# Optimization experiments

Measured on AMD Instinct MI355X. Metric: run time of the kernel, lower is better.

The kernel has to match this reference:

```python
import jax, jax.numpy as jnp
import numpy as np

SCALING = 2.0      # lora_alpha / r = 32 / 16
TEMPERATURE = 1.0  # router_temperature


def setup_inputs() -> dict:
    key = jax.random.key(0)
    ks = jax.random.split(key, 7)
    B, S, D, K, R = 4, 2048, 4096, 8, 16
    # Note: torch inits lora_B to zeros; we use small random values so the
    return {
        "x": jax.random.normal(ks[0], (B, S, D), dtype=jnp.float32),
        "base_w": jax.random.normal(ks[1], (D, D), dtype=jnp.float32) * 0.02,
        "base_b": jax.random.normal(ks[2], (D,), dtype=jnp.float32) * 0.02,
        "lora_A": jax.random.normal(ks[3], (K, R, D), dtype=jnp.float32) * 0.02,
        "lora_B": jax.random.normal(ks[4], (K, D, R), dtype=jnp.float32) * 0.02,
        "router_w": jax.random.normal(ks[5], (K, D), dtype=jnp.float32) * 0.02,
        "router_b": jnp.zeros((K,), dtype=jnp.float32),
    }


def reference(x, base_w, base_b, lora_A, lora_B, router_w, router_b):
    # base_layer(x): x @ W^T + b
    base = jnp.einsum("bsd,od->bso", x, base_w) + base_b
    # router on mean-pooled sequence (x.dim()==3 branch): softmax(Linear(mean_s x))
    router_in = x.mean(axis=1)                                   # [B, D]
    logits = router_in @ router_w.T + router_b                   # [B, K]
    weights = jax.nn.softmax(logits / TEMPERATURE, axis=-1)      # [B, K]
    # grouped LoRA experts: h = A_k x, out = sum_k w_k * B_k h  (dropout p=0 -> identity)
    h = jnp.einsum("bsd,krd->bskr", x, lora_A)                   # [B, S, K, R]
    lora = jnp.einsum("bskr,kor,bk->bso", h, lora_B, weights)    # [B, S, D]
    return base + SCALING * lora
```

## Files before the change

kernel.cpp:

```cpp
#include <hip/hip_runtime.h>
#include <hip/hip_fp16.h>
#include <stdint.h>

typedef _Float16 f16;
typedef __attribute__((ext_vector_type(8))) _Float16 f16x8;
typedef __attribute__((ext_vector_type(4))) float f32x4;

#define D_DIM 4096
#define S_DIM 2048
#define M_DIM 8192
#define R_DIM 16
#define KR 128
#define KTOT 4224
#define SCALING 2.0f

#define WS_AP    0
#define WS_WP    69206016
#define WS_AH    103809024
#define WS_HP    104857600
#define WS_CS    121634816
#define WS_LG    121700352
#define WS_WS    121700480

__device__ __forceinline__ void load_lds16(const void* g, void* l) {
  __builtin_amdgcn_global_load_lds(
      (const __attribute__((address_space(1))) void*)g,
      (__attribute__((address_space(3))) void*)l, 16, 0, 0);
}

union H4 { f16 h[4]; ushort4 u; };

__global__ void conv_x(const float* __restrict__ x, f16* __restrict__ Ap,
                       float* __restrict__ colsum) {
  int rc = blockIdx.x;
  int cc = blockIdx.y;
  int col = cc * 1024 + threadIdx.x * 4;
  long base = (long)rc * 64 * D_DIM + col;
  float s0 = 0, s1 = 0, s2 = 0, s3 = 0;
  for (int r = 0; r < 64; ++r) {
    float4 v = *(const float4*)(x + base + (long)r * D_DIM);
    H4 t; t.h[0] = (f16)v.x; t.h[1] = (f16)v.y; t.h[2] = (f16)v.z; t.h[3] = (f16)v.w;
    *(ushort4*)((char*)Ap + ((long)(rc * 64 + r) * KTOT + col) * 2) = t.u;
    s0 += v.x; s1 += v.y; s2 += v.z; s3 += v.w;
  }
  int b = rc >> 5;
  float* cs = colsum + b * D_DIM + col;
  atomicAdd(cs + 0, s0); atomicAdd(cs + 1, s1);
  atomicAdd(cs + 2, s2); atomicAdd(cs + 3, s3);
}

__global__ void conv_w(const float* __restrict__ w, f16* __restrict__ Wp) {
  int rc = blockIdx.x;
  int cc = blockIdx.y;
  int col = cc * 1024 + threadIdx.x * 4;
  long base = (long)rc * 64 * D_DIM + col;
  for (int r = 0; r < 64; ++r) {
    float4 v = *(const float4*)(w + base + (long)r * D_DIM);
    H4 t; t.h[0] = (f16)v.x; t.h[1] = (f16)v.y; t.h[2] = (f16)v.z; t.h[3] = (f16)v.w;
    *(ushort4*)((char*)Wp + ((long)(rc * 64 + r) * KTOT + col) * 2) = t.u;
  }
}

__global__ void conv_bext(const float* __restrict__ loraB, f16* __restrict__ Wp) {
  int g = blockIdx.x * 256 + threadIdx.x;
  int n = g >> 7, kr = g & 127;
  int k = kr >> 4, r = kr & 15;
  float v = loraB[((long)k * D_DIM + n) * R_DIM + r];
  Wp[(long)n * KTOT + D_DIM + kr] = (f16)v;
}

__global__ void conv_aext(const float* __restrict__ loraA, f16* __restrict__ Ah) {
  long g = ((long)blockIdx.x * 256 + threadIdx.x) * 4;
  float4 v = *(const float4*)(loraA + g);
  H4 t; t.h[0] = (f16)v.x; t.h[1] = (f16)v.y; t.h[2] = (f16)v.z; t.h[3] = (f16)v.w;
  *(ushort4*)((char*)Ah + g * 2) = t.u;
}

__global__ void router_logits(const float* __restrict__ colsum, const float* __restrict__ rw,
                              const float* __restrict__ rb, float* __restrict__ logits) {
  int b = blockIdx.x >> 3, k = blockIdx.x & 7;
  const float* cs = colsum + b * D_DIM;
  const float* w = rw + k * D_DIM;
  float p = 0.f;
  for (int d = threadIdx.x; d < D_DIM; d += 256) p += cs[d] * w[d];
  __shared__ float red[4];
  for (int off = 32; off; off >>= 1) p += __shfl_down(p, off);
  if ((threadIdx.x & 63) == 0) red[threadIdx.x >> 6] = p;
  __syncthreads();
  if (threadIdx.x == 0)
    logits[b * 8 + k] = (red[0] + red[1] + red[2] + red[3]) / (float)S_DIM + rb[k];
}

__global__ void router_softmax(const float* __restrict__ logits, float* __restrict__ wsc) {
  int lane = threadIdx.x;
  if (lane < 32) {
    float L = logits[lane];
    float m = L;
    m = fmaxf(m, __shfl_xor(m, 1));
    m = fmaxf(m, __shfl_xor(m, 2));
    m = fmaxf(m, __shfl_xor(m, 4));
    float e = __expf(L - m);
    float s = e;
    s += __shfl_xor(s, 1); s += __shfl_xor(s, 2); s += __shfl_xor(s, 4);
    wsc[lane] = e / s * SCALING;
  }
}

__global__ void combine_h(const float* __restrict__ hp, const float* __restrict__ wsc,
                          f16* __restrict__ Ap) {
  long g = (long)blockIdx.x * 256 + threadIdx.x;
  long row = g >> 7; int kr = (int)(g & 127);
  int b = (int)(row >> 11);
  float s = hp[g] + hp[g + 1048576] + hp[g + 2097152] + hp[g + 3145728];
  Ap[row * KTOT + D_DIM + kr] = (f16)(s * wsc[b * 8 + (kr >> 4)]);
}

template <int MODE>
__global__ __launch_bounds__(256, 2) void gemm_bt(
    const f16* __restrict__ A, int lda, const f16* __restrict__ Bt, int ldb,
    int kIters, const float* __restrict__ bias, float* __restrict__ C, int ldc) {
  __shared__ __align__(16) f16 As[128 * 64];
  __shared__ __align__(16) f16 Bs[128 * 64];
  int tid = threadIdx.x;
  int wave = tid >> 6, lane = tid & 63;
  long row0 = (long)blockIdx.x * 128;
  long col0 = (long)blockIdx.y * 128;
  int wr = wave >> 1, wc = wave & 1;
  int fr = lane & 15, fq = lane >> 4;
  int srow = lane >> 3;
  int scol = (lane & 7) * 8;
  long koff = (MODE == 2) ? (long)blockIdx.z * 1024 : 0;

  f32x4 acc[4][4] = {};

  for (int kb = 0; kb < kIters; ++kb) {
    long kbase = (long)kb * 64 + koff;
    for (int i = 0; i < 4; ++i) {
      int seg = i * 4 + wave;
      const f16* ga = A + (row0 + seg * 8 + srow) * lda + kbase + scol;
      load_lds16(ga, (char*)As + seg * 1024);
      const f16* gb = Bt + (col0 + seg * 8 + srow) * ldb + kbase + scol;
      load_lds16(gb, (char*)Bs + seg * 1024);
    }
    __syncthreads();
    for (int ks = 0; ks < 2; ++ks) {
      int kbyte = ks * 64 + fq * 16;
      f16x8 af[4], bf[4];
      for (int mi = 0; mi < 4; ++mi)
        af[mi] = *(const f16x8*)((const char*)As + (wr * 64 + mi * 16 + fr) * 128 + kbyte);
      for (int ni = 0; ni < 4; ++ni)
        bf[ni] = *(const f16x8*)((const char*)Bs + (wc * 64 + ni * 16 + fr) * 128 + kbyte);
      for (int mi = 0; mi < 4; ++mi)
        for (int ni = 0; ni < 4; ++ni)
          acc[mi][ni] = __builtin_amdgcn_mfma_f32_16x16x32_f16(af[mi], bf[ni], acc[mi][ni], 0, 0, 0);
    }
    __syncthreads();
  }

  if (MODE == 0) {
    for (int ni = 0; ni < 4; ++ni) {
      long col = col0 + wc * 64 + ni * 16 + fr;
      float bv = bias[col];
      for (int mi = 0; mi < 4; ++mi) {
        long row = row0 + wr * 64 + mi * 16 + fq * 4;
        float* cp = C + row * ldc + col;
        #pragma unroll
        for (int j = 0; j < 4; ++j) cp[(long)j * ldc] = acc[mi][ni][j] + bv;
      }
    }
  } else {
    long zb = (long)blockIdx.z * (long)M_DIM * 128;
    for (int ni = 0; ni < 4; ++ni) {
      int col = wc * 64 + ni * 16 + fr;
      for (int mi = 0; mi < 4; ++mi) {
        long row = row0 + wr * 64 + mi * 16 + fq * 4;
        float* cp = C + zb + row * 128 + col;
        #pragma unroll
        for (int j = 0; j < 4; ++j) cp[(long)j * 128] = acc[mi][ni][j];
      }
    }
  }
}

extern "C" void kernel_launch(void* const* d_in, const int* in_sizes, int n_in,
                              void* d_out, int out_size, void* d_ws, size_t ws_size,
                              hipStream_t stream) {
  (void)in_sizes; (void)n_in; (void)out_size; (void)ws_size;
  const float* x        = (const float*)d_in[0];
  const float* base_w   = (const float*)d_in[1];
  const float* base_b   = (const float*)d_in[2];
  const float* lora_A   = (const float*)d_in[3];
  const float* lora_B   = (const float*)d_in[4];
  const float* router_w = (const float*)d_in[5];
  const float* router_b = (const float*)d_in[6];
  float* out = (float*)d_out;

  char* ws = (char*)d_ws;
  f16* Ap       = (f16*)(ws + WS_AP);
  f16* Wp       = (f16*)(ws + WS_WP);
  f16* Ah       = (f16*)(ws + WS_AH);
  float* hp     = (float*)(ws + WS_HP);
  float* colsum = (float*)(ws + WS_CS);
  float* logits = (float*)(ws + WS_LG);
  float* wsc    = (float*)(ws + WS_WS);

  hipMemsetAsync(colsum, 0, 65536, stream);
  conv_x<<<dim3(128, 4), 256, 0, stream>>>(x, Ap, colsum);
  conv_w<<<dim3(64, 4), 256, 0, stream>>>(base_w, Wp);
  conv_bext<<<2048, 256, 0, stream>>>(lora_B, Wp);
  conv_aext<<<512, 256, 0, stream>>>(lora_A, Ah);
  router_logits<<<32, 256, 0, stream>>>(colsum, router_w, router_b, logits);
  router_softmax<<<1, 64, 0, stream>>>(logits, wsc);
  gemm_bt<2><<<dim3(64, 1, 4), 256, 0, stream>>>(Ap, KTOT, Ah, D_DIM, 16, nullptr, hp, 128);
  combine_h<<<4096, 256, 0, stream>>>(hp, wsc, Ap);
  gemm_bt<0><<<dim3(64, 32), 256, 0, stream>>>(Ap, KTOT, Wp, KTOT, 66, base_b, out, D_DIM);
}
```

Before: 653.5 us.

## Replace base GEMM with 256x256 double-buffered swizzled LDS kernel

```diff
diff --git a/kernel.cpp b/kernel.cpp
--- a/kernel.cpp
+++ b/kernel.cpp
@@ -12,15 +12,16 @@
 #define R_DIM 16
 #define KR 128
 #define KTOT 4224
+#define NKT 66
 #define SCALING 2.0f
 
 #define WS_AP    0
 #define WS_WP    69206016
 #define WS_AH    103809024
 #define WS_HP    104857600
-#define WS_CS    121634816
-#define WS_LG    121700352
-#define WS_WS    121700480
+#define WS_PART  121634816
+#define WS_LG    123731968
+#define WS_WS    123732096
 
 __device__ __forceinline__ void load_lds16(const void* g, void* l) {
   __builtin_amdgcn_global_load_lds(
@@ -31,7 +32,7 @@
 union H4 { f16 h[4]; ushort4 u; };
 
 __global__ void conv_x(const float* __restrict__ x, f16* __restrict__ Ap,
-                       float* __restrict__ colsum) {
+                       float* __restrict__ part) {
   int rc = blockIdx.x;
   int cc = blockIdx.y;
   int col = cc * 1024 + threadIdx.x * 4;
@@ -43,10 +44,8 @@
     *(ushort4*)((char*)Ap + ((long)(rc * 64 + r) * KTOT + col) * 2) = t.u;
     s0 += v.x; s1 += v.y; s2 += v.z; s3 += v.w;
   }
-  int b = rc >> 5;
-  float* cs = colsum + b * D_DIM + col;
-  atomicAdd(cs + 0, s0); atomicAdd(cs + 1, s1);
-  atomicAdd(cs + 2, s2); atomicAdd(cs + 3, s3);
+  float4 sv; sv.x = s0; sv.y = s1; sv.z = s2; sv.w = s3;
+  *(float4*)(part + (long)rc * D_DIM + col) = sv;
 }
 
 __global__ void conv_w(const float* __restrict__ w, f16* __restrict__ Wp) {
@@ -76,13 +75,17 @@
   *(ushort4*)((char*)Ah + g * 2) = t.u;
 }
 
-__global__ void router_logits(const float* __restrict__ colsum, const float* __restrict__ rw,
+__global__ void router_logits(const float* __restrict__ part, const float* __restrict__ rw,
                               const float* __restrict__ rb, float* __restrict__ logits) {
   int b = blockIdx.x >> 3, k = blockIdx.x & 7;
-  const float* cs = colsum + b * D_DIM;
   const float* w = rw + k * D_DIM;
   float p = 0.f;
-  for (int d = threadIdx.x; d < D_DIM; d += 256) p += cs[d] * w[d];
+  for (int d = threadIdx.x; d < D_DIM; d += 256) {
+    float s = 0.f;
+    #pragma unroll 8
+    for (int i = 0; i < 32; ++i) s += part[(long)(b * 32 + i) * D_DIM + d];
+    p += s * w[d];
+  }
   __shared__ float red[4];
   for (int off = 32; off; off >>= 1) p += __shfl_down(p, off);
   if ((threadIdx.x & 63) == 0) red[threadIdx.x >> 6] = p;
@@ -115,21 +118,20 @@
   Ap[row * KTOT + D_DIM + kr] = (f16)(s * wsc[b * 8 + (kr >> 4)]);
 }
 
-template <int MODE>
-__global__ __launch_bounds__(256, 2) void gemm_bt(
+__global__ __launch_bounds__(256, 2) void gemm_h(
     const f16* __restrict__ A, int lda, const f16* __restrict__ Bt, int ldb,
-    int kIters, const float* __restrict__ bias, float* __restrict__ C, int ldc) {
+    int kIters, float* __restrict__ C) {
   __shared__ __align__(16) f16 As[128 * 64];
   __shared__ __align__(16) f16 Bs[128 * 64];
   int tid = threadIdx.x;
   int wave = tid >> 6, lane = tid & 63;
   long row0 = (long)blockIdx.x * 128;
-  long col0 = (long)blockIdx.y * 128;
+  long col0 = 0;
   int wr = wave >> 1, wc = wave & 1;
   int fr = lane & 15, fq = lane >> 4;
   int srow = lane >> 3;
   int scol = (lane & 7) * 8;
-  long koff = (MODE == 2) ? (long)blockIdx.z * 1024 : 0;
+  long koff = (long)blockIdx.z * 1024;
 
   f32x4 acc[4][4] = {};
 
@@ -157,27 +159,108 @@
     __syncthreads();
   }
 
-  if (MODE == 0) {
-    for (int ni = 0; ni < 4; ++ni) {
-      long col = col0 + wc * 64 + ni * 16 + fr;
-      float bv = bias[col];
-      for (int mi = 0; mi < 4; ++mi) {
-        long row = row0 + wr * 64 + mi * 16 + fq * 4;
-        float* cp = C + row * ldc + col;
+  long zb = (long)blockIdx.z * (long)M_DIM * 128;
+  for (int ni = 0; ni < 4; ++ni) {
+    int col = wc * 64 + ni * 16 + fr;
+    for (int mi = 0; mi < 4; ++mi) {
+      long row = row0 + wr * 64 + mi * 16 + fq * 4;
+      float* cp = C + zb + row * 128 + col;
+      #pragma unroll
+      for (int j = 0; j < 4; ++j) cp[(long)j * 128] = acc[mi][ni][j];
+    }
+  }
+}
+
+__device__ __forceinline__ void stage256(const f16* __restrict__ G, long row0, int ld,
+                                         long kbase, char* ldsT, int tid) {
+  int lr = tid >> 3;
+  int sw = (((tid & 7) * 16) ^ ((lr & 7) << 4)) >> 1;
+  char* wbase = ldsT + ((tid >> 6) << 10);
+  #pragma unroll
+  for (int j = 0; j < 4; ++j) {
+    const f16* g = G + (row0 + j * 64 + lr) * (long)ld + kbase + sw;
+    load_lds16(g, wbase + j * 8192);
+  }
+}
+
+__global__ __launch_bounds__(512, 2) void gemm256(
+    const f16* __restrict__ A, int lda, const f16* __restrict__ Bt, int ldb,
+    int nkt, const float* __restrict__ bias, float* __restrict__ C, int ldc) {
+  __shared__ __align__(16) char smem[131072];
+  int tid = threadIdx.x;
+  int wave = tid >> 6, lane = tid & 63;
+  int wr = wave >> 2, wc = wave & 3;
+  int fr = lane & 15, fq = lane >> 4;
+
+  int flat = blockIdx.x;
+  int wg = (flat & 7) * 64 + (flat >> 3);
+  long row0 = (long)(wg >> 4) * 256;
+  long col0 = (long)(wg & 15) * 256;
+
+  f32x4 acc[8][4] = {};
+
+  stage256(A,  row0, lda, 0,  smem,          tid);
+  stage256(Bt, col0, ldb, 0,  smem + 32768,  tid);
+  stage256(A,  row0, lda, 64, smem + 65536,  tid);
+  stage256(Bt, col0, ldb, 64, smem + 98304,  tid);
+  asm volatile("s_waitcnt vmcnt(8)" ::: "memory");
+  asm volatile("s_barrier" ::: "memory");
+
+  int cur = 0;
+  int sw = (fr & 7) << 4;
+  for (int t = 0; t < nkt; ++t) {
+    const char* Ab = smem + cur * 65536;
+    const char* Bb = Ab + 32768;
+    #pragma unroll
+    for (int qm = 0; qm < 2; ++qm) {
+      f16x8 af[4][2];
+      #pragma unroll
+      for (int m2 = 0; m2 < 4; ++m2) {
+        int row = wr * 128 + (qm * 4 + m2) * 16 + fr;
+        af[m2][0] = *(const f16x8*)(Ab + row * 128 + ((fq * 16) ^ sw));
+        af[m2][1] = *(const f16x8*)(Ab + row * 128 + ((64 + fq * 16) ^ sw));
+      }
+      #pragma unroll
+      for (int qn = 0; qn < 2; ++qn) {
+        f16x8 bf[2][2];
         #pragma unroll
-        for (int j = 0; j < 4; ++j) cp[(long)j * ldc] = acc[mi][ni][j] + bv;
+        for (int n2 = 0; n2 < 2; ++n2) {
+          int rowb = wc * 64 + (qn * 2 + n2) * 16 + fr;
+          bf[n2][0] = *(const f16x8*)(Bb + rowb * 128 + ((fq * 16) ^ sw));
+          bf[n2][1] = *(const f16x8*)(Bb + rowb * 128 + ((64 + fq * 16) ^ sw));
+        }
+        #pragma unroll
+        for (int m2 = 0; m2 < 4; ++m2)
+          #pragma unroll
+          for (int n2 = 0; n2 < 2; ++n2) {
+            f32x4* a = &acc[qm * 4 + m2][qn * 2 + n2];
+            *a = __builtin_amdgcn_mfma_f32_16x16x32_f16(af[m2][0], bf[n2][0], *a, 0, 0, 0);
+            *a = __builtin_amdgcn_mfma_f32_16x16x32_f16(af[m2][1], bf[n2][1], *a, 0, 0, 0);
+          }
       }
     }
-  } else {
-    long zb = (long)blockIdx.z * (long)M_DIM * 128;
-    for (int ni = 0; ni < 4; ++ni) {
-      int col = wc * 64 + ni * 16 + fr;
-      for (int mi = 0; mi < 4; ++mi) {
-        long row = row0 + wr * 64 + mi * 16 + fq * 4;
-        float* cp = C + zb + row * 128 + col;
-        #pragma unroll
-        for (int j = 0; j < 4; ++j) cp[(long)j * 128] = acc[mi][ni][j];
-      }
+    asm volatile("s_barrier" ::: "memory");
+    if (t + 2 < nkt) {
+      stage256(A,  row0, lda, (long)(t + 2) * 64, smem + cur * 65536,         tid);
+      stage256(Bt, col0, ldb, (long)(t + 2) * 64, smem + cur * 65536 + 32768, tid);
+      asm volatile("s_waitcnt vmcnt(8)" ::: "memory");
+    } else {
+      asm volatile("s_waitcnt vmcnt(0)" ::: "memory");
+    }
+    asm volatile("s_barrier" ::: "memory");
+    cur ^= 1;
+  }
+
+  #pragma unroll
+  for (int ni = 0; ni < 4; ++ni) {
+    long col = col0 + wc * 64 + ni * 16 + fr;
+    float bv = bias[col];
+    #pragma unroll
+    for (int mi = 0; mi < 8; ++mi) {
+      long row = row0 + wr * 128 + mi * 16 + fq * 4;
+      float* cp = C + row * ldc + col;
+      #pragma unroll
+      for (int j = 0; j < 4; ++j) cp[(long)j * ldc] = acc[mi][ni][j] + bv;
     }
   }
 }
@@ -200,18 +283,17 @@
   f16* Wp       = (f16*)(ws + WS_WP);
   f16* Ah       = (f16*)(ws + WS_AH);
   float* hp     = (float*)(ws + WS_HP);
-  float* colsum = (float*)(ws + WS_CS);
+  float* part   = (float*)(ws + WS_PART);
   float* logits = (float*)(ws + WS_LG);
   float* wsc    = (float*)(ws + WS_WS);
 
-  hipMemsetAsync(colsum, 0, 65536, stream);
-  conv_x<<<dim3(128, 4), 256, 0, stream>>>(x, Ap, colsum);
+  conv_x<<<dim3(128, 4), 256, 0, stream>>>(x, Ap, part);
   conv_w<<<dim3(64, 4), 256, 0, stream>>>(base_w, Wp);
   conv_bext<<<2048, 256, 0, stream>>>(lora_B, Wp);
   conv_aext<<<512, 256, 0, stream>>>(lora_A, Ah);
-  router_logits<<<32, 256, 0, stream>>>(colsum, router_w, router_b, logits);
+  router_logits<<<32, 256, 0, stream>>>(part, router_w, router_b, logits);
   router_softmax<<<1, 64, 0, stream>>>(logits, wsc);
-  gemm_bt<2><<<dim3(64, 1, 4), 256, 0, stream>>>(Ap, KTOT, Ah, D_DIM, 16, nullptr, hp, 128);
+  gemm_h<<<dim3(64, 1, 4), 256, 0, stream>>>(Ap, KTOT, Ah, D_DIM, 16, hp);
   combine_h<<<4096, 256, 0, stream>>>(hp, wsc, Ap);
-  gemm_bt<0><<<dim3(64, 32), 256, 0, stream>>>(Ap, KTOT, Wp, KTOT, 66, base_b, out, D_DIM);
-}
+  gemm256<<<512, 512, 0, stream>>>(Ap, KTOT, Wp, KTOT, NKT, base_b, out, D_DIM);
+}
```

New measurement: 589.0 us. -9.9%, faster.
